# Performance work log

Hardware: AMD Instinct MI355X
Metric: run time of the kernel (lower is better)

## Reference

```python
import jax, jax.numpy as jnp
import numpy as np

N = 100_000   # nodes
E = 3_200_000 # directed edges (avg degree 32)
D = 256       # feature dim (in_channels)
K = 2         # k of k-MIS


def _propagate_min(min_rank, row, col, n, k):
    # k iterations of scatter_min along edges (row -> col), keeping current value
    for _ in range(k):
        neigh = jax.ops.segment_min(min_rank[row], col, num_segments=n)
        min_rank = jnp.minimum(min_rank, neigh)
    return min_rank


def maximal_k_independent_set(row, col, rank, n, k):
    # Luby-style greedy k-MIS: repeatedly add nodes whose rank is minimal in their
    # k-hop in-neighbourhood, then mark (cover) the k-hop neighbourhood of the MIS.
    def dilate(mask):
        for _ in range(k):
            neigh = jax.ops.segment_max(mask[row].astype(jnp.int32), col, num_segments=n)
            mask = mask | (neigh > 0)
        return mask

    def cond(state):
        _, mask, _ = state
        return ~jnp.all(mask)

    def body(state):
        mis, mask, min_rank = state
        min_rank = _propagate_min(min_rank, row, col, n, k)
        mis = mis | (rank == min_rank)
        mask = dilate(mis)
        min_rank = jnp.where(mask, n, rank)  # covered nodes get rank 'infinity' (= n)
        return mis, mask, min_rank

    z = jnp.zeros((n,), dtype=bool)
    mis, _, _ = jax.lax.while_loop(cond, body, (z, z, rank))
    return mis


def cluster_k_mis(mis, row, col, rank, n, k):
    # min_rank = n everywhere except MIS nodes get their rank; propagate min k hops;
    # cluster id = index of the unique MIS rank each node ends up attached to.
    min_rank = jnp.where(mis, rank, n)
    min_rank = _propagate_min(min_rank, row, col, n, k)
    _, clusters = jnp.unique(min_rank, return_inverse=True)
    return clusters.reshape(-1).astype(jnp.int32)


def setup_inputs():
    key = jax.random.key(0)
    k1, k2, k3 = jax.random.split(key, 3)
    x = jax.random.normal(k1, (N, D), dtype=jnp.float32)
    edge_index = jax.random.randint(k2, (2, E), 0, N, dtype=jnp.int32)
    edge_attr = jax.random.normal(k3, (E,), dtype=jnp.float32)
    return {"x": x, "edge_index": edge_index, "edge_attr": edge_attr}


def reference(x, edge_index, edge_attr):
    n = x.shape[0]
    row, col = edge_index[0], edge_index[1]
    # scorer=None -> score = arange(n); greedy ordering of arange -> rank = arange(n)
    rank = jnp.arange(n, dtype=jnp.int32)

    mis = maximal_k_independent_set(row, col, rank, n, K)
    cluster = cluster_k_mis(mis, row, col, rank, n, K)
    c = int(mis.sum())  # number of clusters (MIS size)

    # --- pooled adjacency: coalesce duplicate (cluster[row], cluster[col]) with sum ---
    cl_np = np.asarray(cluster).astype(np.int64)
    r = cl_np[np.asarray(row)]
    cc = cl_np[np.asarray(col)]
    keys = r * np.int64(c) + cc
    uniq, inv = np.unique(keys, return_inverse=True)
    val = jax.ops.segment_sum(edge_attr, jnp.asarray(inv.astype(np.int32)),
                              num_segments=int(uniq.shape[0]))
    new_row = (uniq // c).astype(np.int32)
    new_col = (uniq % c).astype(np.int32)
    keep = np.nonzero(new_row != new_col)[0]  # remove_self_loops=True
    pooled_edge_index = jnp.stack([jnp.asarray(new_row[keep]), jnp.asarray(new_col[keep])])
    pooled_edge_attr = val[jnp.asarray(keep)]

    # --- pooled node features: reduce_x='sum' (adaptive=False, so no score scaling) ---
    x_pooled = jax.ops.segment_sum(x, cluster, num_segments=c)
    return x_pooled, pooled_edge_index, pooled_edge_attr
```

## Files before the change

kernel.cpp:

```cpp
#include <hip/hip_runtime.h>
#include <cmath>
#include <cstdint>

#define NT 256
#define EG0 1024
#define EG1 256
#define MAX_ROUND 16
#define SCAN_T 32
#define SCAN_IPB (NT*SCAN_T)
#define SENT 0x80000000u


__device__ __forceinline__ int getbit(const unsigned int* bm, int v){
  return (bm[v>>5]>>(v&31))&1u;
}
__device__ __forceinline__ void setbit(unsigned int* bm, int v){
  unsigned int m = 1u<<(v&31);
  if(!(bm[v>>5]&m)) atomicOr(&bm[v>>5], m);
}

__device__ __forceinline__ int block_append(int* cursor, bool pred, int* s_w){
  int wid  = threadIdx.x >> 6;
  int lane = threadIdx.x & 63;
  unsigned long long m = __ballot(pred);
  int cnt = __popcll(m);
  if(lane==0) s_w[wid]=cnt;
  __syncthreads();
  if(threadIdx.x==0){
    int t0=s_w[0], t1=s_w[1], t2=s_w[2], t3=s_w[3];
    int tot=t0+t1+t2+t3;
    int base = tot ? atomicAdd(cursor, tot) : 0;
    s_w[0]=base; s_w[1]=base+t0; s_w[2]=base+t0+t1; s_w[3]=base+t0+t1+t2;
  }
  __syncthreads();
  int pos = s_w[wid] + __popcll(m & ((1ull<<lane)-1ull));
  __syncthreads();
  return pos;
}


__global__ void k_init(int* a, int* b, int n){
  int v = blockIdx.x*NT + threadIdx.x;
  if(v<n){ a[v]=v; b[v]=v; }
}

__global__ void k_fill_dense(float* dense, const int* scal, long CMsq){
  long c = scal[0];
  long M = c*c; if(M>CMsq) M=CMsq;
  long stride = (long)gridDim.x*NT;
  for(long i = (long)blockIdx.x*NT + threadIdx.x; i<M; i+=stride)
    ((unsigned int*)dense)[i] = SENT;
}


__global__ void k_hop0(int* b, const int* __restrict__ row,
                       const int* __restrict__ col, int E){
  int stride = gridDim.x*NT;
  for(int e = blockIdx.x*NT + threadIdx.x; e<E; e+=stride){
    int s = row[e];
    if(s < b[col[e]]) atomicMin(&b[col[e]], s);
  }
}

__global__ void k_hop0f(int* a, const int* b, const int* __restrict__ row,
                        const int* __restrict__ col, int n, int E){
  int stride = gridDim.x*NT;
  int total = n + E;
  for(int i = blockIdx.x*NT + threadIdx.x; i<total; i+=stride){
    if(i<n){
      if(b[i] < a[i]) atomicMin(&a[i], b[i]);
    } else {
      int e = i-n;
      int s = b[row[e]];
      if(s < a[col[e]]) atomicMin(&a[col[e]], s);
    }
  }
}

__global__ void k_dil0(const int* a, int* d2, int* cover, const int* __restrict__ row,
                       const int* __restrict__ col, int E, int ep){
  int stride = gridDim.x*NT;
  for(int e = blockIdx.x*NT + threadIdx.x; e<E; e+=stride){
    int r = row[e];
    if(a[r]==r){
      int cc = col[e];
      d2[r]=ep;  cover[r]=1;
      d2[cc]=ep; cover[cc]=1;
    }
  }
}

__global__ void k_dil20(const int* a, const int* d2, int* cover, const int* __restrict__ row,
                        const int* __restrict__ col, int E, int ep){
  int stride = gridDim.x*NT;
  for(int e = blockIdx.x*NT + threadIdx.x; e<E; e+=stride){
    int r = row[e];
    if((d2[r]==ep || a[r]==r) && !cover[col[e]]) cover[col[e]]=1;
  }
}

__global__ void k_fincomp0(int* a, int* b, unsigned int* misb, int* cover, int n,
                           const int* __restrict__ row, const int* __restrict__ col, int E,
                           int2* Ld, int* lcnt1, int* U1, int* rcnt0){
  __shared__ int s_w[4];
  long nth = (long)gridDim.x*NT;
  for(long base = (long)blockIdx.x*NT; base < n; base += nth){
    int v = (int)base + threadIdx.x;
    bool unc = false;
    if(v<n){
      int nw = (a[v]==v);
      if(nw){ setbit(misb,v); if(!cover[v]) cover[v]=1; }
      int cov = cover[v] | nw;
      int val = cov ? n : v;
      a[v]=val; b[v]=val;
      unc = !cov;
    }
    int pos = block_append(rcnt0, unc, s_w);
    if(unc) U1[pos]=v;
  }
  for(long base = (long)blockIdx.x*NT; base < E; base += nth){
    int e = (int)base + threadIdx.x;
    bool keep=false; int2 ed;
    if(e<E){
      ed = make_int2(row[e], col[e]);
      keep = (!cover[ed.x]) || (!cover[ed.y]);
    }
    int pos = block_append(lcnt1, keep, s_w);
    if(keep) Ld[pos]=ed;
  }
}


__global__ void k_hop1(int* b, const int* a, const int2* L, const int* pE,
                       const int* gate){
  if(*gate==0) return;
  int E = *pE;
  int stride = gridDim.x*NT;
  for(int e = blockIdx.x*NT + threadIdx.x; e<E; e+=stride){
    int2 ed = L[e];
    int s = a[ed.x];
    if(s < b[ed.y]) atomicMin(&b[ed.y], s);
  }
}

__global__ void k_hop1f(int* a, const int* b, const int2* L, const int* pE,
                        const int* U, const int* pU, const int* gate){
  if(*gate==0) return;
  int E = *pE, un = *pU;
  int total = un + E;
  int stride = gridDim.x*NT;
  for(int i = blockIdx.x*NT + threadIdx.x; i<total; i+=stride){
    if(i<un){
      int u = U[i];
      if(b[u] < a[u]) atomicMin(&a[u], b[u]);
    } else {
      int2 ed = L[i-un];
      int s = b[ed.x];
      if(s < a[ed.y]) atomicMin(&a[ed.y], s);
    }
  }
}

__global__ void k_dil11(const int* a, int* d2, int* cover, unsigned int* misb,
                        const int2* L, const int* pE, const int* U, const int* pU,
                        const int* gate, int ep){
  if(*gate==0) return;
  int E = *pE, un = *pU;
  int total = un + E;
  int stride = gridDim.x*NT;
  for(int i = blockIdx.x*NT + threadIdx.x; i<total; i+=stride){
    if(i<un){
      int u = U[i];
      if(a[u]==u){ setbit(misb,u); cover[u]=1; d2[u]=ep; }
    } else {
      int2 ed = L[i-un];
      if(a[ed.x]==ed.x){ d2[ed.x]=ep; cover[ed.x]=1; d2[ed.y]=ep; cover[ed.y]=1; }
    }
  }
}

__global__ void k_dil21(const int* a, const int* d2, int* cover, const int2* L,
                        const int* pE, const int* gate, int ep){
  if(*gate==0) return;
  int E = *pE;
  int stride = gridDim.x*NT;
  for(int e = blockIdx.x*NT + threadIdx.x; e<E; e+=stride){
    int2 ed = L[e];
    if((d2[ed.x]==ep || a[ed.x]==ed.x) && !cover[ed.y]) cover[ed.y]=1;
  }
}

__global__ void k_fincomp1(int* a, int* b, const int* cover, int n,
                           const int2* Ls, const int* pE, int2* Ld, int* lcntD,
                           const int* Us, const int* pU, int* Ud, int* rcntD,
                           const int* gate){
  if(*gate==0) return;
  __shared__ int s_w[4];
  int E = *pE, un = *pU;
  long nth = (long)gridDim.x*NT;
  for(long base = (long)blockIdx.x*NT; base < un; base += nth){
    int i = (int)base + threadIdx.x;
    bool unc=false; int u=0;
    if(i<un){ u = Us[i]; unc = !cover[u]; }
    int pos = block_append(rcntD, unc, s_w);
    if(unc) Ud[pos]=u;
  }
  for(long base = (long)blockIdx.x*NT; base < E; base += nth){
    int e = (int)base + threadIdx.x;
    bool keep=false; int2 ed;
    if(e<E){
      ed = Ls[e];
      int vx = cover[ed.x] ? n : ed.x;  a[ed.x]=vx; b[ed.x]=vx;
      int vy = cover[ed.y] ? n : ed.y;  a[ed.y]=vy; b[ed.y]=vy;
      keep = (!cover[ed.x]) || (!cover[ed.y]);
    }
    int pos = block_append(lcntD, keep, s_w);
    if(keep) Ld[pos]=ed;
  }
}


__global__ void k_cluster_init(const unsigned int* misb, unsigned int* reach1b,
                               int* a, int* b, int n){
  int v = blockIdx.x*NT + threadIdx.x;
  if(v<n){
    int m = getbit(misb,v);
    int val = m ? v : n;
    a[v]=val; b[v]=val;
    if(m) setbit(reach1b,v);
  }
}

__global__ void k_chop1(int* b, const unsigned int* misb, unsigned int* reach1b,
                        const int* __restrict__ row, const int* __restrict__ col, int E){
  int stride = gridDim.x*NT;
  for(int e = blockIdx.x*NT + threadIdx.x; e<E; e+=stride){
    int r = row[e];
    if(getbit(misb,r)){
      int cc = col[e];
      if(r < b[cc]) atomicMin(&b[cc], r);
      setbit(reach1b, cc);
    }
  }
}

__global__ void k_chop2f(int* a, const int* b, const unsigned int* reach1b,
                         const int* __restrict__ row, const int* __restrict__ col,
                         int n, int E){
  int stride = gridDim.x*NT;
  int total = n + E;
  for(int i = blockIdx.x*NT + threadIdx.x; i<total; i+=stride){
    if(i<n){
      if(b[i] < a[i]) atomicMin(&a[i], b[i]);
    } else {
      int e = i-n;
      int r = row[e];
      if(getbit(reach1b,r)){
        int s = b[r];
        if(s < n && s < a[col[e]]) atomicMin(&a[col[e]], s);
      }
    }
  }
}

__global__ void k_mark(const int* mr, const unsigned int* misb, int* present, int* cmis, int n){
  int v = blockIdx.x*NT + threadIdx.x;
  int m = 0;
  if(v<n){
    int r = mr[v];
    if(r<n && !present[r]) present[r]=1;
    m = getbit(misb,v);
  }
  __shared__ int sh[NT];
  sh[threadIdx.x]=m; __syncthreads();
  for(int off=NT/2; off>0; off>>=1){
    if(threadIdx.x<off) sh[threadIdx.x]+=sh[threadIdx.x+off];
    __syncthreads();
  }
  if(threadIdx.x==0 && sh[0]) atomicAdd(cmis, sh[0]);
}


__global__ void k_scan1(const int* A, int M, int* bsum){
  int t = threadIdx.x;
  long base = (long)blockIdx.x*SCAN_IPB + (long)t*SCAN_T;
  int s = 0;
  #pragma unroll
  for(int j=0;j<SCAN_T;j++){ long i=base+j; if(i<M) s += A[i]; }
  __shared__ int sh[NT];
  sh[t]=s; __syncthreads();
  for(int off=NT/2; off>0; off>>=1){ if(t<off) sh[t]+=sh[t+off]; __syncthreads(); }
  if(t==0) bsum[blockIdx.x]=sh[0];
}

__global__ void k_scan2(const int* bsum, int* bscan, int B, int* totalOut){
  __shared__ int sh[NT];
  int t = threadIdx.x;
  int carry = 0;
  for(int base=0; base<B; base+=NT){
    int i = base+t;
    int v = (i<B) ? bsum[i] : 0;
    sh[t]=v; __syncthreads();
    for(int off=1; off<NT; off<<=1){
      int x=0; if(t>=off) x=sh[t-off];
      __syncthreads();
      sh[t]+=x; __syncthreads();
    }
    int incl = sh[t];
    if(i<B) bscan[i] = carry + incl - v;
    carry += sh[NT-1];
    __syncthreads();
  }
  if(t==0 && totalOut) *totalOut = carry;
}

__global__ void k_scan3(const int* A, int M, const int* bscan, int* pref){
  int t = threadIdx.x;
  long base = (long)blockIdx.x*SCAN_IPB + (long)t*SCAN_T;
  int s = 0;
  #pragma unroll
  for(int j=0;j<SCAN_T;j++){ long i=base+j; if(i<M) s += A[i]; }
  __shared__ int sh[NT];
  sh[t]=s; __syncthreads();
  for(int off=1; off<NT; off<<=1){
    int x=0; if(t>=off) x=sh[t-off];
    __syncthreads();
    sh[t]+=x; __syncthreads();
  }
  int run = bscan[blockIdx.x] + (sh[t]-s);
  for(int j=0;j<SCAN_T;j++){
    long i=base+j;
    if(i<M){ pref[i]=run; run += A[i]; }
  }
}


__global__ void k_assign(const int* mr, const int* pref, int* cl, int* ccount, int n){
  int v = blockIdx.x*NT + threadIdx.x;
  if(v<n){
    int r = mr[v];
    int cid = (r<n) ? pref[r] : 0;
    cl[v]=cid;
    atomicAdd(&ccount[cid],1);
  }
}

__global__ void k_scatter_nodes(const int* cl, const int* cstart, int* cursor, int* nodeList, int n){
  int v = blockIdx.x*NT + threadIdx.x;
  if(v<n){
    int cid = cl[v];
    int pos = cstart[cid] + atomicAdd(&cursor[cid],1);
    nodeList[pos]=v;
  }
}

__global__ void __launch_bounds__(1024)
k_pool_x(const float* __restrict__ x, const int* nodeList, const int* cstart,
         const int* ccount, const int* scal, float* out, long out_size){
  __shared__ float sh[4][256];
  int c = scal[0], U = scal[1];
  int t = threadIdx.x & 255;
  int g = threadIdx.x >> 8;
  for(int cid=blockIdx.x; cid<c; cid+=gridDim.x){
    float s = 0.f;
    if(cid<U){
      int st = cstart[cid], cn = ccount[cid];
      for(int i=g; i<cn; i+=4)
        s += x[(size_t)nodeList[st+i]*256 + t];
    }
    sh[g][t]=s;
    __syncthreads();
    if(g==0){
      long idx = (long)cid*256 + t;
      if(idx < out_size) out[idx] = sh[0][t]+sh[1][t]+sh[2][t]+sh[3][t];
    }
    __syncthreads();
  }
}

__global__ void k_edge_pool(const int* __restrict__ row, const int* __restrict__ col,
                            const float* __restrict__ attr, const int* cl,
                            const int* scal, float* dense, int E, long CMsq){
  int c = scal[0];
  int stride = gridDim.x*NT;
  for(int e = blockIdx.x*NT + threadIdx.x; e<E; e+=stride){
    long key = (long)cl[row[e]]*c + cl[col[e]];
    if(key < CMsq){
      unsafeAtomicAdd(&dense[key], attr[e]);
    }
  }
}

__device__ __forceinline__ int cellp(const float* dense, long i){
  return __float_as_uint(dense[i]) != SENT;
}

__global__ void k_cscan1(const float* dense, const int* scal, int* bsum, long CMsq){
  int c = scal[0];
  long M = (long)c*c; if(M>CMsq) M=CMsq;
  int t = threadIdx.x;
  long base = (long)blockIdx.x*SCAN_IPB + (long)t*SCAN_T;
  int s = 0;
  if(base < M && c > 0){
    int r = (int)(base / c);
    int q = (int)(base - (long)r*c);
    for(int j=0;j<SCAN_T;j++){
      long i=base+j;
      if(i<M){
        if(cellp(dense,i) && r!=q) s++;
      }
      if(++q==c){ q=0; r++; }
    }
  }
  __shared__ int sh[NT];
  sh[t]=s; __syncthreads();
  for(int off=NT/2; off>0; off>>=1){ if(t<off) sh[t]+=sh[t+off]; __syncthreads(); }
  if(t==0) bsum[blockIdx.x]=sh[0];
}

__global__ void k_cemit(const float* dense, const int* scal,
                        const int* bscan, float* out, long out_size, long CMsq){
  int c = scal[0]; int P = scal[2];
  long M = (long)c*c; if(M>CMsq) M=CMsq;
  long xoff = (long)c*256;
  int t = threadIdx.x;
  long base = (long)blockIdx.x*SCAN_IPB + (long)t*SCAN_T;
  int s = 0;
  int r0=0,q0=0;
  if(base < M && c > 0){
    r0 = (int)(base / c);
    q0 = (int)(base - (long)r0*c);
    int r=r0, q=q0;
    for(int j=0;j<SCAN_T;j++){
      long i=base+j;
      if(i<M){
        if(cellp(dense,i) && r!=q) s++;
      }
      if(++q==c){ q=0; r++; }
    }
  }
  __shared__ int sh[NT];
  sh[t]=s; __syncthreads();
  for(int off=1; off<NT; off<<=1){
    int x=0; if(t>=off) x=sh[t-off];
    __syncthreads();
    sh[t]+=x; __syncthreads();
  }
  int run = bscan[blockIdx.x] + (sh[t]-s);
  if(base < M && c > 0){
    int r=r0, q=q0;
    for(int j=0;j<SCAN_T;j++){
      long i=base+j;
      if(i<M && cellp(dense,i) && r!=q){
        long o0 = xoff + run;
        long o1 = xoff + (long)P + run;
        long o2 = xoff + 2L*(long)P + run;
        if(o0<out_size) out[o0]=(float)r;
        if(o1<out_size) out[o1]=(float)q;
        if(o2<out_size) out[o2]=dense[i];
        run++;
      }
      if(++q==c){ q=0; r++; }
    }
  }
}


extern "C" void kernel_launch(void* const* d_in, const int* in_sizes, int n_in,
                              void* d_out, int out_size, void* d_ws, size_t ws_size,
                              hipStream_t stream){
  (void)n_in;
  const float* x     = (const float*)d_in[0];
  const int*   eidx  = (const int*)d_in[1];
  const float* eattr = (const float*)d_in[2];
  const int D = 256;
  int n = in_sizes[0]/D;
  int E = in_sizes[1]/2;
  const int* row = eidx;
  const int* col = eidx + E;
  int nwords = (n+31)>>5;
  int CU_B = out_size/256 + 1; if(CU_B > n) CU_B = n;

  char* p = (char*)d_ws;
  auto alloc = [&](size_t bytes)->char*{ char* r=p; p += (bytes+255)&~(size_t)255; return r; };
  int2* LA   = (int2*)alloc((size_t)E*8);
  int2* LB   = (int2*)alloc((size_t)E*8);
  int* a     = (int*)alloc((size_t)n*4);
  int* b     = (int*)alloc((size_t)n*4);
  int* cl    = (int*)alloc((size_t)n*4);
  int* nodeList = (int*)alloc((size_t)n*4);
  int* pref  = (int*)alloc((size_t)n*4);
  int* U1    = (int*)alloc((size_t)n*4);
  int* U2    = (int*)alloc((size_t)n*4);
  int* bsum  = (int*)alloc(4096*4);
  int* bscan = (int*)alloc(4096*4);
  char* zstart = p;
  int* cover   = (int*)alloc((size_t)n*4);
  int* d2      = (int*)alloc((size_t)n*4);
  unsigned int* misb    = (unsigned int*)alloc((size_t)nwords*4);
  unsigned int* reach1b = (unsigned int*)alloc((size_t)nwords*4);
  int* present = (int*)alloc((size_t)n*4);
  int* ccount  = (int*)alloc((size_t)n*4);
  int* cursor  = (int*)alloc((size_t)n*4);
  int* rcnt    = (int*)alloc((MAX_ROUND+2)*4);
  int* lcnt    = (int*)alloc((MAX_ROUND+2)*4);
  int* scal    = (int*)alloc(64);
  size_t zbytes = (size_t)(p - zstart);

  size_t used   = (size_t)(p-(char*)d_ws);
  size_t remain = (ws_size > used+4096) ? ws_size-used-4096 : 0;
  size_t cells  = remain/4;
  long CM = (long)std::sqrt((double)cells);
  while(CM>1 && CM*CM > (long)cells) CM--;
  if(CM>4096) CM=4096;
  if(CM<1) CM=1;
  long CMsq = CM*CM;
  float* dense = (float*)alloc((size_t)CMsq*4);

  hipMemsetAsync(zstart, 0, zbytes, stream);

  int NB  = (n+NT-1)/NT;
  int NBs = (n+SCAN_IPB-1)/SCAN_IPB;
  int NBc = (CU_B+SCAN_IPB-1)/SCAN_IPB;
  int CB  = (int)((CMsq+SCAN_IPB-1)/SCAN_IPB);

  k_init    <<<NB,NT,0,stream>>>(a,b,n);
  k_hop0    <<<EG0,NT,0,stream>>>(b,row,col,E);
  k_hop0f   <<<EG0,NT,0,stream>>>(a,b,row,col,n,E);
  k_dil0    <<<EG0,NT,0,stream>>>(a,d2,cover,row,col,E,1);
  k_dil20   <<<EG0,NT,0,stream>>>(a,d2,cover,row,col,E,1);
  k_fincomp0<<<EG0,NT,0,stream>>>(a,b,misb,cover,n,row,col,E,LB,&lcnt[1],U1,&rcnt[0]);

  for(int r=1; r<MAX_ROUND; ++r){
    int2* Ls = (r&1) ? LB : LA;
    int2* Ld = (r&1) ? LA : LB;
    int*  Us = (r&1) ? U1 : U2;
    int*  Ud = (r&1) ? U2 : U1;
    int ep = r+1;
    k_hop1    <<<EG1,NT,0,stream>>>(b,a,Ls,&lcnt[r],&rcnt[r-1]);
    k_hop1f   <<<EG1,NT,0,stream>>>(a,b,Ls,&lcnt[r],Us,&rcnt[r-1],&rcnt[r-1]);
    k_dil11   <<<EG1,NT,0,stream>>>(a,d2,cover,misb,Ls,&lcnt[r],Us,&rcnt[r-1],&rcnt[r-1],ep);
    k_dil21   <<<EG1,NT,0,stream>>>(a,d2,cover,Ls,&lcnt[r],&rcnt[r-1],ep);
    k_fincomp1<<<EG1,NT,0,stream>>>(a,b,cover,n,Ls,&lcnt[r],Ld,&lcnt[r+1],
                                    Us,&rcnt[r-1],Ud,&rcnt[r],&rcnt[r-1]);
  }

  k_cluster_init<<<NB,NT,0,stream>>>(misb,reach1b,a,b,n);
  k_chop1 <<<EG0,NT,0,stream>>>(b,misb,reach1b,row,col,E);
  k_chop2f<<<EG0,NT,0,stream>>>(a,b,reach1b,row,col,n,E);

  k_mark <<<NB,NT,0,stream>>>(a,misb,present,scal,n);
  k_scan1<<<NBs,NT,0,stream>>>(present,n,bsum);
  k_scan2<<<1,NT,0,stream>>>(bsum,bscan,NBs,scal+1);
  k_scan3<<<NBs,NT,0,stream>>>(present,n,bscan,pref);
  k_assign<<<NB,NT,0,stream>>>(a,pref,cl,ccount,n);

  k_fill_dense<<<2048,NT,0,stream>>>(dense,scal,CMsq);

  k_scan1<<<NBc,NT,0,stream>>>(ccount,CU_B,bsum);
  k_scan2<<<1,NT,0,stream>>>(bsum,bscan,NBc,nullptr);
  k_scan3<<<NBc,NT,0,stream>>>(ccount,CU_B,bscan,pref);
  k_scatter_nodes<<<NB,NT,0,stream>>>(cl,pref,cursor,nodeList,n);

  k_pool_x<<<1024,1024,0,stream>>>(x,nodeList,pref,ccount,scal,(float*)d_out,(long)out_size);

  k_edge_pool<<<EG0,NT,0,stream>>>(row,col,eattr,cl,scal,dense,E,CMsq);
  k_cscan1<<<CB,NT,0,stream>>>(dense,scal,bsum,CMsq);
  k_scan2 <<<1,NT,0,stream>>>(bsum,bscan,CB,scal+2);
  k_cemit <<<CB,NT,0,stream>>>(dense,scal,bscan,(float*)d_out,(long)out_size,CMsq);
}
```

Before: 1.933 ms.

## Privatize pooled-edge atomics into multiple dense copies and simplify node-feature pooling

Edge pooling now scatters atomics into four private copies of the dense cluster-pair matrix, chosen by block index. A new reduction kernel sums the copies before the compaction scan; the intent is to cut atomic contention on hot cells. The node-feature pooling kernel drops from 1024 to 256 threads per block, replacing shared-memory group reduction with four independent register accumulators per thread. The dense buffer is now sized from CU_B under a tighter memory budget, and the scan grid is capped at 4096 blocks. This adds extra fill and reduce traffic and reduces thread-level parallelism per cluster in feature pooling.

New measurement: 1.823 ms. 5.7% less time.

```diff
diff --git a/kernel.cpp b/kernel.cpp
--- a/kernel.cpp
+++ b/kernel.cpp
@@ -6,6 +6,7 @@
 #define EG0 1024
 #define EG1 256
 #define MAX_ROUND 16
+#define KCOPY 4
 #define SCAN_T 32
 #define SCAN_IPB (NT*SCAN_T)
 #define SENT 0x80000000u
@@ -44,12 +45,15 @@
   if(v<n){ a[v]=v; b[v]=v; }
 }
 
-__global__ void k_fill_dense(float* dense, const int* scal, long CMsq){
+__global__ void k_fill_dense(float* dcopies, const int* scal, long CMsq){
   long c = scal[0];
   long M = c*c; if(M>CMsq) M=CMsq;
   long stride = (long)gridDim.x*NT;
-  for(long i = (long)blockIdx.x*NT + threadIdx.x; i<M; i+=stride)
-    ((unsigned int*)dense)[i] = SENT;
+  for(long i = (long)blockIdx.x*NT + threadIdx.x; i<M; i+=stride){
+    #pragma unroll
+    for(int k=0;k<KCOPY;k++)
+      ((unsigned int*)dcopies)[(long)k*CMsq + i] = SENT;
+  }
 }
 
 
@@ -354,40 +358,54 @@
   }
 }
 
-__global__ void __launch_bounds__(1024)
-k_pool_x(const float* __restrict__ x, const int* nodeList, const int* cstart,
-         const int* ccount, const int* scal, float* out, long out_size){
-  __shared__ float sh[4][256];
+__global__ void k_pool_x(const float* __restrict__ x, const int* nodeList, const int* cstart,
+                         const int* ccount, const int* scal, float* out, long out_size){
   int c = scal[0], U = scal[1];
-  int t = threadIdx.x & 255;
-  int g = threadIdx.x >> 8;
+  int t = threadIdx.x;
   for(int cid=blockIdx.x; cid<c; cid+=gridDim.x){
-    float s = 0.f;
+    float s0=0.f, s1=0.f, s2=0.f, s3=0.f;
     if(cid<U){
       int st = cstart[cid], cn = ccount[cid];
-      for(int i=g; i<cn; i+=4)
-        s += x[(size_t)nodeList[st+i]*256 + t];
-    }
-    sh[g][t]=s;
-    __syncthreads();
-    if(g==0){
-      long idx = (long)cid*256 + t;
-      if(idx < out_size) out[idx] = sh[0][t]+sh[1][t]+sh[2][t]+sh[3][t];
-    }
-    __syncthreads();
+      int i=0;
+      for(; i+3<cn; i+=4){
+        int n0=nodeList[st+i], n1=nodeList[st+i+1], n2=nodeList[st+i+2], n3=nodeList[st+i+3];
+        s0 += x[(size_t)n0*256 + t];
+        s1 += x[(size_t)n1*256 + t];
+        s2 += x[(size_t)n2*256 + t];
+        s3 += x[(size_t)n3*256 + t];
+      }
+      for(; i<cn; i++) s0 += x[(size_t)nodeList[st+i]*256 + t];
+      s0 += s1+s2+s3;
+    }
+    long idx = (long)cid*256 + t;
+    if(idx < out_size) out[idx]=s0;
   }
 }
 
 __global__ void k_edge_pool(const int* __restrict__ row, const int* __restrict__ col,
                             const float* __restrict__ attr, const int* cl,
-                            const int* scal, float* dense, int E, long CMsq){
+                            const int* scal, float* dcopies, int E, long CMsq){
   int c = scal[0];
+  float* dc = dcopies + (long)(blockIdx.x & (KCOPY-1))*CMsq;
   int stride = gridDim.x*NT;
   for(int e = blockIdx.x*NT + threadIdx.x; e<E; e+=stride){
     long key = (long)cl[row[e]]*c + cl[col[e]];
     if(key < CMsq){
-      unsafeAtomicAdd(&dense[key], attr[e]);
-    }
+      unsafeAtomicAdd(&dc[key], attr[e]);
+    }
+  }
+}
+
+__global__ void k_reduce_dense(const float* __restrict__ dcopies, float* dense,
+                               const int* scal, long CMsq){
+  long c = scal[0];
+  long M = c*c; if(M>CMsq) M=CMsq;
+  long stride = (long)gridDim.x*NT;
+  for(long i = (long)blockIdx.x*NT + threadIdx.x; i<M; i+=stride){
+    float s = dcopies[i];
+    #pragma unroll
+    for(int k=1;k<KCOPY;k++) s += dcopies[(long)k*CMsq + i];
+    dense[i]=s;
   }
 }
 
@@ -509,13 +527,12 @@
 
   size_t used   = (size_t)(p-(char*)d_ws);
   size_t remain = (ws_size > used+4096) ? ws_size-used-4096 : 0;
-  size_t cells  = remain/4;
-  long CM = (long)std::sqrt((double)cells);
-  while(CM>1 && CM*CM > (long)cells) CM--;
-  if(CM>4096) CM=4096;
-  if(CM<1) CM=1;
+  size_t maxcells = remain/(4*(KCOPY+1));
+  long CM = CU_B;
+  while(CM>1 && (size_t)CM*CM > maxcells) CM--;
   long CMsq = CM*CM;
-  float* dense = (float*)alloc((size_t)CMsq*4);
+  float* dcopies = (float*)alloc((size_t)KCOPY*CMsq*4);
+  float* dense   = (float*)alloc((size_t)CMsq*4);
 
   hipMemsetAsync(zstart, 0, zbytes, stream);
 
@@ -523,6 +540,7 @@
   int NBs = (n+SCAN_IPB-1)/SCAN_IPB;
   int NBc = (CU_B+SCAN_IPB-1)/SCAN_IPB;
   int CB  = (int)((CMsq+SCAN_IPB-1)/SCAN_IPB);
+  if(CB>4096) CB=4096;
 
   k_init    <<<NB,NT,0,stream>>>(a,b,n);
   k_hop0    <<<EG0,NT,0,stream>>>(b,row,col,E);
@@ -555,16 +573,17 @@
   k_scan3<<<NBs,NT,0,stream>>>(present,n,bscan,pref);
   k_assign<<<NB,NT,0,stream>>>(a,pref,cl,ccount,n);
 
-  k_fill_dense<<<2048,NT,0,stream>>>(dense,scal,CMsq);
+  k_fill_dense<<<2048,NT,0,stream>>>(dcopies,scal,CMsq);
 
   k_scan1<<<NBc,NT,0,stream>>>(ccount,CU_B,bsum);
   k_scan2<<<1,NT,0,stream>>>(bsum,bscan,NBc,nullptr);
   k_scan3<<<NBc,NT,0,stream>>>(ccount,CU_B,bscan,pref);
   k_scatter_nodes<<<NB,NT,0,stream>>>(cl,pref,cursor,nodeList,n);
 
-  k_pool_x<<<1024,1024,0,stream>>>(x,nodeList,pref,ccount,scal,(float*)d_out,(long)out_size);
-
-  k_edge_pool<<<EG0,NT,0,stream>>>(row,col,eattr,cl,scal,dense,E,CMsq);
+  k_pool_x<<<1024,NT,0,stream>>>(x,nodeList,pref,ccount,scal,(float*)d_out,(long)out_size);
+
+  k_edge_pool<<<EG0,NT,0,stream>>>(row,col,eattr,cl,scal,dcopies,E,CMsq);
+  k_reduce_dense<<<1024,NT,0,stream>>>(dcopies,dense,scal,CMsq);
   k_cscan1<<<CB,NT,0,stream>>>(dense,scal,bsum,CMsq);
   k_scan2 <<<1,NT,0,stream>>>(bsum,bscan,CB,scal+2);
   k_cemit <<<CB,NT,0,stream>>>(dense,scal,bscan,(float*)d_out,(long)out_size,CMsq);
```
